# Optimization experiments

Measured on AMD Instinct MI355X. Metric: run time of the kernel, lower is better.

## Reference

```python
import jax, jax.numpy as jnp
import numpy as np

BLOCK = 32  # GGUF Q8_0 block size


def setup_inputs() -> dict:
    key = jax.random.key(0)
    k1, k2, k3, k4 = jax.random.split(key, 4)
    O, I = 11008, 4096
    x = jax.random.normal(k1, (32, I), dtype=jnp.float32)
    qweight = jax.random.randint(k2, (O, I), 0, 255, dtype=jnp.int32)
    scales = jax.random.uniform(k3, (O, I // BLOCK), dtype=jnp.float32) * 0.01
    bias = jax.random.normal(k4, (O,), dtype=jnp.float32)
    return {"x": x, "qweight": qweight, "scales": scales, "bias": bias}


def dequantize(qweight, scales):
    # Q8_0-style: signed int8 quants, one fp scale per block of 32 along in-dim.
    O, I = qweight.shape
    q = (qweight.astype(scales.dtype) - 127.0).reshape(O, I // BLOCK, BLOCK)
    w = q * scales[:, :, None]  # [O, nb, BLOCK]
    return w.reshape(O, I)


def reference(x, qweight, scales, bias):
    # On-the-fly dequant fused with F.linear: y = x @ W^T + b
    w = dequantize(qweight, scales)           # [O, I]
    return jnp.einsum('bi,oi->bo', x, w) + bias
```

## Files before the change

### kernel.cpp

```cpp
#include <hip/hip_runtime.h>
#include <hip/hip_bf16.h>


#define O_DIM  11008
#define I_DIM  4096
#define NB     128
#define B_DIM  32
#define NSPLIT 32
#define KT     (I_DIM / NSPLIT)
#define PART_STRIDE (O_DIM * B_DIM)

typedef __attribute__((ext_vector_type(8))) short bf16x8;
typedef __attribute__((ext_vector_type(8))) unsigned short u16x8;
typedef __attribute__((ext_vector_type(4))) float f32x4;
typedef __attribute__((ext_vector_type(4))) int   i32x4;

static __device__ __forceinline__ unsigned short f2bf(float f) {
    return __builtin_bit_cast(unsigned short, __float2bfloat16(f));
}

static __device__ __forceinline__ unsigned int pkf16(float a, float b) {
    const unsigned short ua = __builtin_bit_cast(unsigned short, (_Float16)a);
    const unsigned short ub = __builtin_bit_cast(unsigned short, (_Float16)b);
    return (unsigned int)ua | ((unsigned int)ub << 16);
}

static __device__ __forceinline__ void gl_lds16(const void* g, void* l) {
    __builtin_amdgcn_global_load_lds(
        (const __attribute__((address_space(1))) void*)g,
        (__attribute__((address_space(3))) void*)l,
        16, 0, 0);
}

static __device__ __forceinline__ bf16x8 dequant8(const i32x4 qa, const i32x4 qb,
                                                  const float s) {
    const float c = -127.0f * s;
    bf16x8 v;
    v[0] = (short)f2bf(fmaf((float)qa[0], s, c));
    v[1] = (short)f2bf(fmaf((float)qa[1], s, c));
    v[2] = (short)f2bf(fmaf((float)qa[2], s, c));
    v[3] = (short)f2bf(fmaf((float)qa[3], s, c));
    v[4] = (short)f2bf(fmaf((float)qb[0], s, c));
    v[5] = (short)f2bf(fmaf((float)qb[1], s, c));
    v[6] = (short)f2bf(fmaf((float)qb[2], s, c));
    v[7] = (short)f2bf(fmaf((float)qb[3], s, c));
    return v;
}

__global__ __launch_bounds__(256) void gemm_kernel(const float* __restrict__ x,
                                                   const int*   __restrict__ qw,
                                                   const float* __restrict__ scales,
                                                   unsigned short* __restrict__ part) {
    __shared__ int            w_s[64 * KT];
    __shared__ unsigned short x_s[B_DIM * KT];

    const int t    = threadIdx.x;
    const int wav  = t >> 6;
    const int lan  = t & 63;
    const int lrow = lan & 15;
    const int lq   = lan >> 4;

    const int split  = blockIdx.x;
    const int k_base = split * KT;
    const int o_wave = blockIdx.y * 64 + wav * 16;
    const int o_row  = o_wave + lrow;

    {
        const int  half = lan >> 5;
        const int  li   = lan & 31;
        char*       ldsb = (char*)w_s + wav * 8192;
        const char* gb   = (const char*)(qw + (size_t)o_wave * I_DIM + k_base);
#pragma unroll
        for (int j = 0; j < 8; ++j) {
            const int rl  = 2 * j + half;
            const int off = (li * 16) ^ ((rl & 7) << 4);
            gl_lds16(gb + (size_t)rl * (I_DIM * 4) + off, ldsb + j * 1024);
        }
    }

    const float4 scv = *reinterpret_cast<const float4*>(&scales[o_row * NB + split * 4]);
    const float sc[4] = {scv.x, scv.y, scv.z, scv.w};

    {
        const int m  = t >> 3;
        const int k0 = (t & 7) * 16;
        const float4* xv = reinterpret_cast<const float4*>(x + m * I_DIM + k_base + k0);
#pragma unroll
        for (int j = 0; j < 2; ++j) {
            const float4 va = xv[2 * j];
            const float4 vb = xv[2 * j + 1];
            bf16x8 v;
            v[0] = (short)f2bf(va.x); v[1] = (short)f2bf(va.y);
            v[2] = (short)f2bf(va.z); v[3] = (short)f2bf(va.w);
            v[4] = (short)f2bf(vb.x); v[5] = (short)f2bf(vb.y);
            v[6] = (short)f2bf(vb.z); v[7] = (short)f2bf(vb.w);
            const int addr = ((m * KT + k0 + j * 8) * 2) ^ ((m & 7) << 4);
            *reinterpret_cast<bf16x8*>(reinterpret_cast<char*>(x_s) + addr) = v;
        }
    }

    __syncthreads();

    f32x4 acc0 = {0.f, 0.f, 0.f, 0.f};
    f32x4 acc1 = {0.f, 0.f, 0.f, 0.f};
    const int swz = (lrow & 7) << 4;
    const char* wbase = (const char*)w_s + wav * 8192 + lrow * 512;
    const char* xbase = (const char*)x_s;

#pragma unroll
    for (int ks = 0; ks < 4; ++ks) {
        const int off = ks * 128 + lq * 32;
        const i32x4 qlo = *reinterpret_cast<const i32x4*>(wbase + ((off)      ^ swz));
        const i32x4 qhi = *reinterpret_cast<const i32x4*>(wbase + ((off + 16) ^ swz));
        const int kb2 = (ks * 32 + lq * 8) * 2;
        const bf16x8 a0 = *reinterpret_cast<const bf16x8*>(
            xbase + (( lrow       * 256 + kb2) ^ swz));
        const bf16x8 a1 = *reinterpret_cast<const bf16x8*>(
            xbase + (((lrow + 16) * 256 + kb2) ^ swz));
        const bf16x8 bf = dequant8(qlo, qhi, sc[ks]);
        acc0 = __builtin_amdgcn_mfma_f32_16x16x32_bf16(a0, bf, acc0, 0, 0, 0);
        acc1 = __builtin_amdgcn_mfma_f32_16x16x32_bf16(a1, bf, acc1, 0, 0, 0);
    }

    unsigned short* pp = part + (size_t)split * PART_STRIDE + o_row * B_DIM;
    const uint2 v0 = make_uint2(pkf16(acc0[0], acc0[1]), pkf16(acc0[2], acc0[3]));
    const uint2 v1 = make_uint2(pkf16(acc1[0], acc1[1]), pkf16(acc1[2], acc1[3]));
    *reinterpret_cast<uint2*>(&pp[lq * 4])      = v0;
    *reinterpret_cast<uint2*>(&pp[16 + lq * 4]) = v1;
}

__global__ __launch_bounds__(256) void reduce_kernel(const unsigned short* __restrict__ part,
                                                     const float* __restrict__ bias,
                                                     float* __restrict__ out) {
    const int o = blockIdx.x * 256 + threadIdx.x;
    float v[B_DIM];
#pragma unroll
    for (int m = 0; m < B_DIM; ++m) v[m] = 0.f;

    for (int s = 0; s < NSPLIT; ++s) {
        const unsigned short* ps = part + (size_t)s * PART_STRIDE + o * B_DIM;
#pragma unroll
        for (int g = 0; g < 4; ++g) {
            const u16x8 p = *reinterpret_cast<const u16x8*>(ps + g * 8);
#pragma unroll
            for (int j = 0; j < 8; ++j)
                v[g * 8 + j] += (float)__builtin_bit_cast(_Float16, (unsigned short)p[j]);
        }
    }

    const float b = bias[o];
#pragma unroll
    for (int m = 0; m < B_DIM; ++m)
        out[m * O_DIM + o] = v[m] + b;
}

extern "C" void kernel_launch(void* const* d_in, const int* in_sizes, int n_in,
                              void* d_out, int out_size, void* d_ws, size_t ws_size,
                              hipStream_t stream) {
    const float* x      = (const float*)d_in[0];
    const int*   qw     = (const int*)d_in[1];
    const float* scales = (const float*)d_in[2];
    const float* bias   = (const float*)d_in[3];
    float*       out    = (float*)d_out;
    unsigned short* part = (unsigned short*)d_ws;

    hipLaunchKernelGGL(gemm_kernel, dim3(NSPLIT, O_DIM / 64), dim3(256), 0, stream,
                       x, qw, scales, part);

    hipLaunchKernelGGL(reduce_kernel, dim3(O_DIM / 256), dim3(256), 0, stream,
                       part, bias, out);
}
```

Measured before the change: 49.93 us.

## Pre-convert x to bf16 and double-buffer weight staging with fewer K splits

Adds a separate kernel that converts x to bf16 once, so the GEMM no longer repeats the fp32-to-bf16 conversion in every block. The GEMM now uses 128-thread blocks where each wave owns a 16-row tile across a 512-wide K slice. It streams the weights through double-buffered LDS using global_load_lds with explicit vmcnt waits, and loads x fragments straight from global into registers. Cutting the K splits from 32 to 8 shrinks the partial buffer and the reduction traffic. The costs are an extra kernel launch and fewer blocks with longer serial work each.

```diff
diff --git a/kernel.cpp b/kernel.cpp
--- a/kernel.cpp
+++ b/kernel.cpp
@@ -6,8 +6,7 @@
 #define I_DIM  4096
 #define NB     128
 #define B_DIM  32
-#define NSPLIT 32
-#define KT     (I_DIM / NSPLIT)
+#define NSG    8
 #define PART_STRIDE (O_DIM * B_DIM)
 
 typedef __attribute__((ext_vector_type(8))) short bf16x8;
@@ -18,20 +17,17 @@
 static __device__ __forceinline__ unsigned short f2bf(float f) {
     return __builtin_bit_cast(unsigned short, __float2bfloat16(f));
 }
-
 static __device__ __forceinline__ unsigned int pkf16(float a, float b) {
     const unsigned short ua = __builtin_bit_cast(unsigned short, (_Float16)a);
     const unsigned short ub = __builtin_bit_cast(unsigned short, (_Float16)b);
     return (unsigned int)ua | ((unsigned int)ub << 16);
 }
-
 static __device__ __forceinline__ void gl_lds16(const void* g, void* l) {
     __builtin_amdgcn_global_load_lds(
         (const __attribute__((address_space(1))) void*)g,
         (__attribute__((address_space(3))) void*)l,
         16, 0, 0);
 }
-
 static __device__ __forceinline__ bf16x8 dequant8(const i32x4 qa, const i32x4 qb,
                                                   const float s) {
     const float c = -127.0f * s;
@@ -47,84 +43,124 @@
     return v;
 }
 
-__global__ __launch_bounds__(256) void gemm_kernel(const float* __restrict__ x,
+__global__ __launch_bounds__(256) void convert_kernel(const float* __restrict__ x,
+                                                      unsigned short* __restrict__ xbf) {
+    const int gid = blockIdx.x * 256 + threadIdx.x;
+    const float4 v = reinterpret_cast<const float4*>(x)[gid];
+    ushort4 u;
+    u.x = f2bf(v.x); u.y = f2bf(v.y); u.z = f2bf(v.z); u.w = f2bf(v.w);
+    reinterpret_cast<ushort4*>(xbf)[gid] = u;
+}
+
+#define SBAR __builtin_amdgcn_sched_barrier(0)
+#define WAITV8 { asm volatile("s_waitcnt vmcnt(8)" ::: "memory"); SBAR; }
+#define WAITV0 { asm volatile("s_waitcnt vmcnt(0)" ::: "memory"); SBAR; }
+#define WAITL  { asm volatile("s_waitcnt lgkmcnt(0)" ::: "memory"); SBAR; }
+
+__global__ __launch_bounds__(128) void gemm_kernel(const unsigned short* __restrict__ xbf,
                                                    const int*   __restrict__ qw,
                                                    const float* __restrict__ scales,
                                                    unsigned short* __restrict__ part) {
-    __shared__ int            w_s[64 * KT];
-    __shared__ unsigned short x_s[B_DIM * KT];
+    __shared__ int w_s[2][2][2048];
 
     const int t    = threadIdx.x;
     const int wav  = t >> 6;
     const int lan  = t & 63;
     const int lrow = lan & 15;
     const int lq   = lan >> 4;
-
-    const int split  = blockIdx.x;
-    const int k_base = split * KT;
-    const int o_wave = blockIdx.y * 64 + wav * 16;
-    const int o_row  = o_wave + lrow;
-
+    const int half = lan >> 5;
+    const int li   = lan & 31;
+
+    const int item   = blockIdx.x * 2 + wav;
+    const int o_tile = item >> 3;
+    const int sg     = item & 7;
+    const int o_base = o_tile * 16;
+    const int o_row  = o_base + lrow;
+    const int k0     = sg * 512;
+
+    float sc[16];
     {
-        const int  half = lan >> 5;
-        const int  li   = lan & 31;
-        char*       ldsb = (char*)w_s + wav * 8192;
-        const char* gb   = (const char*)(qw + (size_t)o_wave * I_DIM + k_base);
-#pragma unroll
-        for (int j = 0; j < 8; ++j) {
-            const int rl  = 2 * j + half;
-            const int off = (li * 16) ^ ((rl & 7) << 4);
-            gl_lds16(gb + (size_t)rl * (I_DIM * 4) + off, ldsb + j * 1024);
+        const float4* sp = reinterpret_cast<const float4*>(&scales[o_row * NB + sg * 16]);
+#pragma unroll
+        for (int j = 0; j < 4; ++j) {
+            const float4 v = sp[j];
+            sc[4*j] = v.x; sc[4*j+1] = v.y; sc[4*j+2] = v.z; sc[4*j+3] = v.w;
         }
     }
-
-    const float4 scv = *reinterpret_cast<const float4*>(&scales[o_row * NB + split * 4]);
-    const float sc[4] = {scv.x, scv.y, scv.z, scv.w};
-
-    {
-        const int m  = t >> 3;
-        const int k0 = (t & 7) * 16;
-        const float4* xv = reinterpret_cast<const float4*>(x + m * I_DIM + k_base + k0);
-#pragma unroll
-        for (int j = 0; j < 2; ++j) {
-            const float4 va = xv[2 * j];
-            const float4 vb = xv[2 * j + 1];
-            bf16x8 v;
-            v[0] = (short)f2bf(va.x); v[1] = (short)f2bf(va.y);
-            v[2] = (short)f2bf(va.z); v[3] = (short)f2bf(va.w);
-            v[4] = (short)f2bf(vb.x); v[5] = (short)f2bf(vb.y);
-            v[6] = (short)f2bf(vb.z); v[7] = (short)f2bf(vb.w);
-            const int addr = ((m * KT + k0 + j * 8) * 2) ^ ((m & 7) << 4);
-            *reinterpret_cast<bf16x8*>(reinterpret_cast<char*>(x_s) + addr) = v;
-        }
-    }
-
-    __syncthreads();
-
-    f32x4 acc0 = {0.f, 0.f, 0.f, 0.f};
-    f32x4 acc1 = {0.f, 0.f, 0.f, 0.f};
+    const unsigned short* xa = xbf + lrow * I_DIM + k0 + lq * 8;
+
+    bf16x8 xe0,xe1,xe2,xe3,xe4,xe5,xe6,xe7;
+    bf16x8 xo0,xo1,xo2,xo3,xo4,xo5,xo6,xo7;
+
+#define LOADX(P, c) { \
+    const unsigned short* xp = xa + (c) * 128; \
+    P##0 = *(const bf16x8*)(xp);       P##1 = *(const bf16x8*)(xp + 16*I_DIM); \
+    P##2 = *(const bf16x8*)(xp + 32);  P##3 = *(const bf16x8*)(xp + 32 + 16*I_DIM); \
+    P##4 = *(const bf16x8*)(xp + 64);  P##5 = *(const bf16x8*)(xp + 64 + 16*I_DIM); \
+    P##6 = *(const bf16x8*)(xp + 96);  P##7 = *(const bf16x8*)(xp + 96 + 16*I_DIM); }
+
+    const char* wsrc = (const char*)qw + ((size_t)o_base * I_DIM + k0) * 4;
+
+#define STAGE(c, buf) { SBAR; { \
+    char* dst = (char*)&w_s[wav][buf][0]; \
+    const char* src = wsrc + (c) * 512; \
+    _Pragma("unroll") \
+    for (int j = 0; j < 8; ++j) { \
+        const int rl  = 2*j + half; \
+        const int off = (li*16) ^ ((rl & 7) << 4); \
+        gl_lds16(src + (size_t)rl * (I_DIM*4) + off, dst + j*1024); \
+    } } SBAR; }
+
+    i32x4 q0,q1,q2,q3,q4,q5,q6,q7;
     const int swz = (lrow & 7) << 4;
-    const char* wbase = (const char*)w_s + wav * 8192 + lrow * 512;
-    const char* xbase = (const char*)x_s;
-
-#pragma unroll
-    for (int ks = 0; ks < 4; ++ks) {
-        const int off = ks * 128 + lq * 32;
-        const i32x4 qlo = *reinterpret_cast<const i32x4*>(wbase + ((off)      ^ swz));
-        const i32x4 qhi = *reinterpret_cast<const i32x4*>(wbase + ((off + 16) ^ swz));
-        const int kb2 = (ks * 32 + lq * 8) * 2;
-        const bf16x8 a0 = *reinterpret_cast<const bf16x8*>(
-            xbase + (( lrow       * 256 + kb2) ^ swz));
-        const bf16x8 a1 = *reinterpret_cast<const bf16x8*>(
-            xbase + (((lrow + 16) * 256 + kb2) ^ swz));
-        const bf16x8 bf = dequant8(qlo, qhi, sc[ks]);
-        acc0 = __builtin_amdgcn_mfma_f32_16x16x32_bf16(a0, bf, acc0, 0, 0, 0);
-        acc1 = __builtin_amdgcn_mfma_f32_16x16x32_bf16(a1, bf, acc1, 0, 0, 0);
-    }
-
-    unsigned short* pp = part + (size_t)split * PART_STRIDE + o_row * B_DIM;
-    const uint2 v0 = make_uint2(pkf16(acc0[0], acc0[1]), pkf16(acc0[2], acc0[3]));
-    const uint2 v1 = make_uint2(pkf16(acc1[0], acc1[1]), pkf16(acc1[2], acc1[3]));
+
+#define DSRD(buf) { \
+    const char* rb = (const char*)&w_s[wav][buf][0] + lrow * 512; \
+    q0 = *(const i32x4*)(rb + ((  0 + lq*32     ) ^ swz)); \
+    q1 = *(const i32x4*)(rb + ((  0 + lq*32 + 16) ^ swz)); \
+    q2 = *(const i32x4*)(rb + ((128 + lq*32     ) ^ swz)); \
+    q3 = *(const i32x4*)(rb + ((128 + lq*32 + 16) ^ swz)); \
+    q4 = *(const i32x4*)(rb + ((256 + lq*32     ) ^ swz)); \
+    q5 = *(const i32x4*)(rb + ((256 + lq*32 + 16) ^ swz)); \
+    q6 = *(const i32x4*)(rb + ((384 + lq*32     ) ^ swz)); \
+    q7 = *(const i32x4*)(rb + ((384 + lq*32 + 16) ^ swz)); }
+
+#define MFMA __builtin_amdgcn_mfma_f32_16x16x32_bf16
+#define COMP(P, cc) { bf16x8 bb; \
+    bb = dequant8(q0,q1,sc[(cc)*4+0]); acc0 = MFMA(P##0,bb,acc0,0,0,0); acc1 = MFMA(P##1,bb,acc1,0,0,0); \
+    bb = dequant8(q2,q3,sc[(cc)*4+1]); acc0 = MFMA(P##2,bb,acc0,0,0,0); acc1 = MFMA(P##3,bb,acc1,0,0,0); \
+    bb = dequant8(q4,q5,sc[(cc)*4+2]); acc0 = MFMA(P##4,bb,acc0,0,0,0); acc1 = MFMA(P##5,bb,acc1,0,0,0); \
+    bb = dequant8(q6,q7,sc[(cc)*4+3]); acc0 = MFMA(P##6,bb,acc0,0,0,0); acc1 = MFMA(P##7,bb,acc1,0,0,0); }
+
+    f32x4 acc0 = {0.f,0.f,0.f,0.f};
+    f32x4 acc1 = {0.f,0.f,0.f,0.f};
+
+    LOADX(xe, 0)
+    STAGE(0, 0)
+    STAGE(1, 1)
+    WAITV8
+    LOADX(xo, 1)
+    DSRD(0)
+    WAITL
+    STAGE(2, 0)
+    COMP(xe, 0)
+    WAITV8
+    LOADX(xe, 2)
+    DSRD(1)
+    WAITL
+    STAGE(3, 1)
+    COMP(xo, 1)
+    WAITV8
+    LOADX(xo, 3)
+    DSRD(0)
+    COMP(xe, 2)
+    WAITV0
+    DSRD(1)
+    COMP(xo, 3)
+
+    unsigned short* pp = part + (size_t)sg * PART_STRIDE + (size_t)o_row * B_DIM;
+    const uint2 v0 = make_uint2(pkf16(acc0[0],acc0[1]), pkf16(acc0[2],acc0[3]));
+    const uint2 v1 = make_uint2(pkf16(acc1[0],acc1[1]), pkf16(acc1[2],acc1[3]));
     *reinterpret_cast<uint2*>(&pp[lq * 4])      = v0;
     *reinterpret_cast<uint2*>(&pp[16 + lq * 4]) = v1;
 }
@@ -137,8 +173,9 @@
 #pragma unroll
     for (int m = 0; m < B_DIM; ++m) v[m] = 0.f;
 
-    for (int s = 0; s < NSPLIT; ++s) {
-        const unsigned short* ps = part + (size_t)s * PART_STRIDE + o * B_DIM;
+#pragma unroll
+    for (int s = 0; s < NSG; ++s) {
+        const unsigned short* ps = part + (size_t)s * PART_STRIDE + (size_t)o * B_DIM;
 #pragma unroll
         for (int g = 0; g < 4; ++g) {
             const u16x8 p = *reinterpret_cast<const u16x8*>(ps + g * 8);
@@ -162,10 +199,14 @@
     const float* scales = (const float*)d_in[2];
     const float* bias   = (const float*)d_in[3];
     float*       out    = (float*)d_out;
-    unsigned short* part = (unsigned short*)d_ws;
-
-    hipLaunchKernelGGL(gemm_kernel, dim3(NSPLIT, O_DIM / 64), dim3(256), 0, stream,
-                       x, qw, scales, part);
+
+    unsigned short* xbf  = (unsigned short*)d_ws;
+    unsigned short* part = (unsigned short*)((char*)d_ws + 262144);
+
+    hipLaunchKernelGGL(convert_kernel, dim3(128), dim3(256), 0, stream, x, xbf);
+
+    hipLaunchKernelGGL(gemm_kernel, dim3(2752), dim3(128), 0, stream,
+                       xbf, qw, scales, part);
 
     hipLaunchKernelGGL(reduce_kernel, dim3(O_DIM / 256), dim3(256), 0, stream,
                        part, bias, out);
```

Result: no change. 49.50 us (-0.9%).
